# Optimization experiments

Hardware: AMD Instinct MI355X
Metric: run time of the kernel (lower is better)

Reference implementation:

```python
import jax, jax.numpy as jnp
import numpy as np

B, N, ATTR, H, OUT, STEPS = 8, 4096, 16, 64, 1, 8


def setup_inputs() -> dict:
    key = jax.random.key(0)
    ks = jax.random.split(key, 12)
    attr_matrix = jax.random.normal(ks[0], (B, N, ATTR), jnp.float32)
    adj_matrix = (jax.random.uniform(ks[1], (B, N, N)) < 0.01).astype(jnp.float32)
    s = float(1.0 / np.sqrt(H))
    u = lambda k, shape: jax.random.uniform(k, shape, jnp.float32, -s, s)
    Wi = jax.random.normal(ks[2], (H, ATTR), jnp.float32) * float(np.sqrt(2.0 / ATTR))  # kaiming
    bi = jnp.zeros((H,), jnp.float32)
    Wz = u(ks[3], (H, 3 * H)); bz = u(ks[4], (H,))
    Wr = u(ks[5], (H, 3 * H)); br = u(ks[6], (H,))
    Wh = u(ks[7], (H, 3 * H)); bh = u(ks[8], (H,))
    Wo = jax.random.normal(ks[9], (OUT, H), jnp.float32) * float(np.sqrt(2.0 / (H + OUT)))  # xavier
    bo = jnp.zeros((OUT,), jnp.float32)
    return dict(attr_matrix=attr_matrix, adj_matrix=adj_matrix, Wi=Wi, bi=bi,
                Wz=Wz, bz=bz, Wr=Wr, br=br, Wh=Wh, bh=bh, Wo=Wo, bo=bo)


def reference(attr_matrix, adj_matrix, Wi, bi, Wz, bz, Wr, br, Wh, bh, Wo, bo):
    # initial node states: (B, N, H)
    h = jax.nn.relu(attr_matrix @ Wi.T + bi)
    A_in = adj_matrix
    A_out = jnp.swapaxes(adj_matrix, -1, -2)
    for _ in range(STEPS):
        a_in = jnp.einsum('bij,bjh->bih', A_in, h)
        a_out = jnp.einsum('bij,bjh->bih', A_out, h)
        inp = jnp.concatenate([a_in, a_out], axis=-1)           # (B, N, 2H)
        xs = jnp.concatenate([inp, h], axis=-1)                  # (B, N, 3H)
        z = jax.nn.sigmoid(xs @ Wz.T + bz)
        r = jax.nn.sigmoid(xs @ Wr.T + br)
        hn = jnp.tanh(jnp.concatenate([inp, r * h], axis=-1) @ Wh.T + bh)
        h = (1.0 - z) * h + z * hn
    return h @ Wo.T + bo  # (B, N, OUT)
```

## Files before the change

kernel.cpp:

```cpp
#include <hip/hip_runtime.h>
#include <hip/hip_fp16.h>
#include <stdint.h>

#define BB 8
#define NN 4096
#define ATTRD 16
#define HD 64
#define STEPS 8
#define NODES (BB*NN)
#define ECAP 96
#define KPAD 196

typedef _Float16 half8 __attribute__((ext_vector_type(8)));
typedef float floatx4 __attribute__((ext_vector_type(4)));
typedef unsigned long long ull;

__global__ void init_h_kernel(const float* __restrict__ attr, const float* __restrict__ Wi,
                              const float* __restrict__ bi, float* __restrict__ h,
                              __half* __restrict__ h16) {
    int idx = blockIdx.x * blockDim.x + threadIdx.x;
    if (idx >= (NODES + 1) * HD) return;
    if (idx >= NODES * HD) {
        h16[idx] = __float2half(0.f);
        return;
    }
    int node = idx >> 6, l = idx & 63;
    const float* a = attr + node * ATTRD;
    const float* w = Wi + l * ATTRD;
    float acc = bi[l];
#pragma unroll
    for (int k = 0; k < ATTRD; k++) acc += a[k] * w[k];
    float r = acc > 0.f ? acc : 0.f;
    h[idx] = r;
    h16[idx] = __float2half(r);
}

__global__ void wprep_kernel(const float* __restrict__ Wz, const float* __restrict__ Wr,
                             const float* __restrict__ Wh,
                             _Float16* __restrict__ wf_hi, _Float16* __restrict__ wf_lo) {
    int t = blockIdx.x * blockDim.x + threadIdx.x;
    if (t >= 3 * 4 * 6 * 64 * 8) return;
    int mat = t / 12288, rem = t % 12288;
    int tile = rem / 3072, rem2 = rem % 3072;
    int kc = rem2 / 512, rem3 = rem2 % 512;
    int lane = rem3 / 8, j = rem3 % 8;
    int k = kc * 32 + (lane >> 4) * 8 + j;
    int och = tile * 16 + (lane & 15);
    const float* W = (mat == 0) ? Wz : (mat == 1) ? Wr : Wh;
    float v = W[och * 192 + k];
    _Float16 hi = (_Float16)v;
    wf_hi[t] = hi;
    wf_lo[t] = (_Float16)(v - (float)hi);
}

__global__ __launch_bounds__(256) void count_rows_kernel(const float4* __restrict__ A4,
                                                         int* __restrict__ cnt_in,
                                                         int* __restrict__ edge_in) {
    int wave = threadIdx.x >> 6, l = threadIdx.x & 63;
    int row = blockIdx.x * 4 + wave;
    const float4* rp = A4 + (size_t)row * 1024;
    ull mask_lt = (l == 63) ? ~0ull >> 1 : ((1ull << (l + 1)) - 1) >> 1;
    float4 v[16];
#pragma unroll
    for (int t = 0; t < 16; t++) v[t] = rp[t * 64 + l];
    int colbase = (row >> 12) << 12;
    int run = 0;
    int* erow = edge_in + row * ECAP;
#pragma unroll
    for (int t = 0; t < 16; t++) {
        ull b0 = __ballot(v[t].x != 0.f);
        ull b1 = __ballot(v[t].y != 0.f);
        ull b2 = __ballot(v[t].z != 0.f);
        ull b3 = __ballot(v[t].w != 0.f);
        int pre = __popcll(b0 & mask_lt) + __popcll(b1 & mask_lt) +
                  __popcll(b2 & mask_lt) + __popcll(b3 & mask_lt);
        float vv[4] = {v[t].x, v[t].y, v[t].z, v[t].w};
        int jbase = (t * 64 + l) * 4;
        int inner = 0;
#pragma unroll
        for (int q = 0; q < 4; q++) {
            if (vv[q] != 0.f) {
                int slot = run + pre + inner;
                if (slot < ECAP) erow[slot] = colbase | (jbase + q);
                inner++;
            }
        }
        run += __popcll(b0) + __popcll(b1) + __popcll(b2) + __popcll(b3);
    }
    if (l == 0) cnt_in[row] = run;
}

__global__ __launch_bounds__(256) void transpose_kernel(const int* __restrict__ cnt_in,
                                                        const int* __restrict__ edge_in,
                                                        int* __restrict__ cnt_out,
                                                        int* __restrict__ edge_out) {
    int wave = threadIdx.x >> 6, l = threadIdx.x & 63;
    int row = blockIdx.x * 4 + wave;
    int n = cnt_in[row]; if (n > ECAP) n = ECAP;
    for (int s = l; s < n; s += 64) {
        int j = edge_in[row * ECAP + s];
        int s2 = atomicAdd(&cnt_out[j], 1);
        if (s2 < ECAP) edge_out[j * ECAP + s2] = row;
    }
}

__global__ __launch_bounds__(256) void aggregate_kernel(
        const uint4* __restrict__ h4, const float* __restrict__ h,
        const int* __restrict__ cnt_in, const int* __restrict__ edge_in,
        const int* __restrict__ cnt_out, const int* __restrict__ edge_out,
        float* __restrict__ xs) {
    int bid = blockIdx.x;
    int batch = bid & 7;
    int group = bid >> 3;
    int wave = threadIdx.x >> 6;
    int pair = group * 4 + wave;
    int node = (batch << 12) + (pair >> 1);
    int dir = pair & 1;
    int l = threadIdx.x & 63;
    int sub = l >> 3;
    int part = l & 7;
    int n = dir ? cnt_out[node] : cnt_in[node];
    if (n > ECAP) n = ECAP;
    const int* erow = (dir ? edge_out : edge_in) + node * ECAP;
    int e0 = erow[l];
    int e1 = erow[64 + (l & 31)];
    float a0 = 0.f, a1 = 0.f, a2 = 0.f, a3 = 0.f, a4 = 0.f, a5 = 0.f, a6 = 0.f, a7 = 0.f;
    for (int s = 0; s < n; s += 8) {
        int il = s + sub;
        int gidx = (il < 64) ? __shfl(e0, il) : __shfl(e1, il - 64);
        gidx = (il < n) ? gidx : NODES;
        uint4 g = h4[(gidx << 3) | part];
        float2 p0 = __half22float2(*(__half2*)&g.x);
        float2 p1 = __half22float2(*(__half2*)&g.y);
        float2 p2 = __half22float2(*(__half2*)&g.z);
        float2 p3 = __half22float2(*(__half2*)&g.w);
        a0 += p0.x; a1 += p0.y; a2 += p1.x; a3 += p1.y;
        a4 += p2.x; a5 += p2.y; a6 += p3.x; a7 += p3.y;
    }
#pragma unroll
    for (int off = 8; off < 64; off <<= 1) {
        a0 += __shfl_xor(a0, off); a1 += __shfl_xor(a1, off);
        a2 += __shfl_xor(a2, off); a3 += __shfl_xor(a3, off);
        a4 += __shfl_xor(a4, off); a5 += __shfl_xor(a5, off);
        a6 += __shfl_xor(a6, off); a7 += __shfl_xor(a7, off);
    }
    if (l < 8) {
        float4 s0 = {a0, a1, a2, a3};
        float4 s1 = {a4, a5, a6, a7};
        float* dst = xs + node * 192 + dir * 64 + l * 8;
        *(float4*)dst = s0;
        *(float4*)(dst + 4) = s1;
    }
    if (dir == 0) xs[node * 192 + 128 + l] = h[(node << 6) | l];
}

__global__ __launch_bounds__(256) void gate_kernel(
        const float* __restrict__ xs_g,
        const _Float16* __restrict__ wf_hi, const _Float16* __restrict__ wf_lo,
        const float* __restrict__ bz, const float* __restrict__ br,
        const float* __restrict__ bh,
        float* __restrict__ h, __half* __restrict__ h16) {
    __shared__ float xs_t[16][KPAD];
    int bid = blockIdx.x;
    int base = ((bid & 7) << 12) | ((bid >> 3) << 4);
    int tid = threadIdx.x;
    {
        const float4* src = (const float4*)(xs_g + base * 192);
#pragma unroll
        for (int i = 0; i < 3; i++) {
            int idx = tid + i * 256;
            float4 v = src[idx];
            int nl = idx / 48, kb = (idx % 48) * 4;
            *(float4*)&xs_t[nl][kb] = v;
        }
    }
    __syncthreads();
    int wave = tid >> 6, lane = tid & 63;
    int m = lane & 15, q = lane >> 4;
    int ch = wave * 16 + m;
    const half8* WH = (const half8*)wf_hi;
    const half8* WL = (const half8*)wf_lo;

    floatx4 accz = {0.f, 0.f, 0.f, 0.f};
    floatx4 accr = {0.f, 0.f, 0.f, 0.f};
#pragma unroll
    for (int kc = 0; kc < 6; kc++) {
        const float* xr = &xs_t[m][kc * 32 + q * 8];
        float4 xa = *(const float4*)xr;
        float4 xb = *(const float4*)(xr + 4);
        float xv[8] = {xa.x, xa.y, xa.z, xa.w, xb.x, xb.y, xb.z, xb.w};
        half8 ahi, alo;
#pragma unroll
        for (int j = 0; j < 8; j++) {
            _Float16 hj = (_Float16)xv[j];
            ahi[j] = hj;
            alo[j] = (_Float16)(xv[j] - (float)hj);
        }
        half8 bzh = WH[((0 * 4 + wave) * 6 + kc) * 64 + lane];
        half8 bzl = WL[((0 * 4 + wave) * 6 + kc) * 64 + lane];
        half8 brh = WH[((1 * 4 + wave) * 6 + kc) * 64 + lane];
        half8 brl = WL[((1 * 4 + wave) * 6 + kc) * 64 + lane];
        accz = __builtin_amdgcn_mfma_f32_16x16x32_f16(ahi, bzh, accz, 0, 0, 0);
        accz = __builtin_amdgcn_mfma_f32_16x16x32_f16(alo, bzh, accz, 0, 0, 0);
        accz = __builtin_amdgcn_mfma_f32_16x16x32_f16(ahi, bzl, accz, 0, 0, 0);
        accr = __builtin_amdgcn_mfma_f32_16x16x32_f16(ahi, brh, accr, 0, 0, 0);
        accr = __builtin_amdgcn_mfma_f32_16x16x32_f16(alo, brh, accr, 0, 0, 0);
        accr = __builtin_amdgcn_mfma_f32_16x16x32_f16(ahi, brl, accr, 0, 0, 0);
    }
    float bzv = bz[ch], brv = br[ch], bhv = bh[ch];
    float zreg[4], hvreg[4], rh[4];
#pragma unroll
    for (int rg = 0; rg < 4; rg++) {
        int nl = q * 4 + rg;
        float z = 1.f / (1.f + __expf(-(accz[rg] + bzv)));
        float r = 1.f / (1.f + __expf(-(accr[rg] + brv)));
        float hv = xs_t[nl][128 + ch];
        zreg[rg] = z; hvreg[rg] = hv; rh[rg] = r * hv;
    }
    __syncthreads();
#pragma unroll
    for (int rg = 0; rg < 4; rg++) xs_t[q * 4 + rg][128 + ch] = rh[rg];
    __syncthreads();

    floatx4 acch = {0.f, 0.f, 0.f, 0.f};
#pragma unroll
    for (int kc = 0; kc < 6; kc++) {
        const float* xr = &xs_t[m][kc * 32 + q * 8];
        float4 xa = *(const float4*)xr;
        float4 xb = *(const float4*)(xr + 4);
        float xv[8] = {xa.x, xa.y, xa.z, xa.w, xb.x, xb.y, xb.z, xb.w};
        half8 ahi, alo;
#pragma unroll
        for (int j = 0; j < 8; j++) {
            _Float16 hj = (_Float16)xv[j];
            ahi[j] = hj;
            alo[j] = (_Float16)(xv[j] - (float)hj);
        }
        half8 bhh = WH[((2 * 4 + wave) * 6 + kc) * 64 + lane];
        half8 bhl = WL[((2 * 4 + wave) * 6 + kc) * 64 + lane];
        acch = __builtin_amdgcn_mfma_f32_16x16x32_f16(ahi, bhh, acch, 0, 0, 0);
        acch = __builtin_amdgcn_mfma_f32_16x16x32_f16(alo, bhh, acch, 0, 0, 0);
        acch = __builtin_amdgcn_mfma_f32_16x16x32_f16(ahi, bhl, acch, 0, 0, 0);
    }
    __syncthreads();
#pragma unroll
    for (int rg = 0; rg < 4; rg++) {
        int nl = q * 4 + rg;
        float pre = acch[rg] + bhv;
        float th = 2.f / (1.f + __expf(-2.f * pre)) - 1.f;
        float hv = hvreg[rg];
        xs_t[nl][ch] = hv + zreg[rg] * (th - hv);
    }
    __syncthreads();
    {
        int f = tid * 4;
        int nl = f >> 6, c = f & 63;
        float4 v = *(const float4*)&xs_t[nl][c];
        int gi = ((base + nl) << 6) | c;
        *(float4*)&h[gi] = v;
        __half2 p0 = {__float2half(v.x), __float2half(v.y)};
        __half2 p1 = {__float2half(v.z), __float2half(v.w)};
        *(__half2*)&h16[gi] = p0;
        *(__half2*)&h16[gi + 2] = p1;
    }
}

__global__ void out_kernel(const float* __restrict__ h, const float* __restrict__ Wo,
                           const float* __restrict__ bo, float* __restrict__ out) {
    int wid = (blockIdx.x * blockDim.x + threadIdx.x) >> 6;
    int l = threadIdx.x & 63;
    if (wid >= NODES) return;
    float p = h[(wid << 6) | l] * Wo[l];
#pragma unroll
    for (int off = 32; off > 0; off >>= 1) p += __shfl_down(p, off);
    if (l == 0) out[wid] = p + bo[0];
}

extern "C" void kernel_launch(void* const* d_in, const int* in_sizes, int n_in,
                              void* d_out, int out_size, void* d_ws, size_t ws_size,
                              hipStream_t stream) {
    const float* attr = (const float*)d_in[0];
    const float* adj  = (const float*)d_in[1];
    const float* Wi   = (const float*)d_in[2];
    const float* bi   = (const float*)d_in[3];
    const float* Wz   = (const float*)d_in[4];
    const float* bz   = (const float*)d_in[5];
    const float* Wr   = (const float*)d_in[6];
    const float* br   = (const float*)d_in[7];
    const float* Wh   = (const float*)d_in[8];
    const float* bh   = (const float*)d_in[9];
    const float* Wo   = (const float*)d_in[10];
    const float* bo   = (const float*)d_in[11];
    float* out = (float*)d_out;

    char* ws = (char*)d_ws;
    size_t off = 0;
    auto carve = [&](size_t bytes) { void* p = ws + off; off = (off + bytes + 255) & ~(size_t)255; return p; };
    float* h      = (float*)carve((size_t)NODES * HD * 4);
    __half* h16   = (__half*)carve((size_t)(NODES + 1) * HD * 2);
    float* xs     = (float*)carve((size_t)NODES * 192 * 4);
    _Float16* wf_hi = (_Float16*)carve(3 * 4 * 6 * 64 * 8 * 2);
    _Float16* wf_lo = (_Float16*)carve(3 * 4 * 6 * 64 * 8 * 2);
    int* cnt_in   = (int*)carve((size_t)NODES * 4);
    int* cnt_out  = (int*)carve((size_t)NODES * 4);
    int* edge_in  = (int*)carve((size_t)NODES * ECAP * 4);
    int* edge_out = (int*)carve((size_t)NODES * ECAP * 4);

    hipMemsetAsync(cnt_out, 0, (size_t)NODES * 4, stream);

    init_h_kernel<<<((NODES + 1) * HD + 255) / 256, 256, 0, stream>>>(attr, Wi, bi, h, h16);
    wprep_kernel<<<(3 * 4 * 6 * 64 * 8 + 255) / 256, 256, 0, stream>>>(Wz, Wr, Wh, wf_hi, wf_lo);
    count_rows_kernel<<<NODES / 4, 256, 0, stream>>>((const float4*)adj, cnt_in, edge_in);
    transpose_kernel<<<NODES / 4, 256, 0, stream>>>(cnt_in, edge_in, cnt_out, edge_out);

    for (int step = 0; step < STEPS; ++step) {
        aggregate_kernel<<<NODES * 2 * 64 / 256, 256, 0, stream>>>(
            (const uint4*)h16, h, cnt_in, edge_in, cnt_out, edge_out, xs);
        gate_kernel<<<NODES / 16, 256, 0, stream>>>(xs, wf_hi, wf_lo, bz, br, bh, h, h16);
    }
    out_kernel<<<NODES * HD / 256, 256, 0, stream>>>(h, Wo, bo, out);
}
```

Baseline: 1.225 ms.

## Fuse adjacency transpose into row scan and merge in/out aggregation per wave

The separate transpose kernel is removed: the row-scan kernel now issues the atomic increments that build the outgoing edge lists directly while it scans the dense adjacency. The aggregate kernel now handles both directions for a node in one wave, interleaving the two gathers and halving the grid. This saves a launch and a re-read of edge lists, and raises memory-level parallelism per wave, at the cost of more registers and idle lanes when in/out degrees differ.

```diff
diff --git a/kernel.cpp b/kernel.cpp
--- a/kernel.cpp
+++ b/kernel.cpp
@@ -55,7 +55,9 @@
 
 __global__ __launch_bounds__(256) void count_rows_kernel(const float4* __restrict__ A4,
                                                          int* __restrict__ cnt_in,
-                                                         int* __restrict__ edge_in) {
+                                                         int* __restrict__ edge_in,
+                                                         int* __restrict__ cnt_out,
+                                                         int* __restrict__ edge_out) {
     int wave = threadIdx.x >> 6, l = threadIdx.x & 63;
     int row = blockIdx.x * 4 + wave;
     const float4* rp = A4 + (size_t)row * 1024;
@@ -80,28 +82,17 @@
 #pragma unroll
         for (int q = 0; q < 4; q++) {
             if (vv[q] != 0.f) {
+                int col = colbase | (jbase + q);
                 int slot = run + pre + inner;
-                if (slot < ECAP) erow[slot] = colbase | (jbase + q);
+                if (slot < ECAP) erow[slot] = col;
                 inner++;
+                int s2 = atomicAdd(&cnt_out[col], 1);
+                if (s2 < ECAP) edge_out[col * ECAP + s2] = row;
             }
         }
         run += __popcll(b0) + __popcll(b1) + __popcll(b2) + __popcll(b3);
     }
     if (l == 0) cnt_in[row] = run;
-}
-
-__global__ __launch_bounds__(256) void transpose_kernel(const int* __restrict__ cnt_in,
-                                                        const int* __restrict__ edge_in,
-                                                        int* __restrict__ cnt_out,
-                                                        int* __restrict__ edge_out) {
-    int wave = threadIdx.x >> 6, l = threadIdx.x & 63;
-    int row = blockIdx.x * 4 + wave;
-    int n = cnt_in[row]; if (n > ECAP) n = ECAP;
-    for (int s = l; s < n; s += 64) {
-        int j = edge_in[row * ECAP + s];
-        int s2 = atomicAdd(&cnt_out[j], 1);
-        if (s2 < ECAP) edge_out[j * ECAP + s2] = row;
-    }
 }
 
 __global__ __launch_bounds__(256) void aggregate_kernel(
@@ -113,45 +104,63 @@
     int batch = bid & 7;
     int group = bid >> 3;
     int wave = threadIdx.x >> 6;
-    int pair = group * 4 + wave;
-    int node = (batch << 12) + (pair >> 1);
-    int dir = pair & 1;
+    int node = (batch << 12) + group * 4 + wave;
     int l = threadIdx.x & 63;
     int sub = l >> 3;
     int part = l & 7;
-    int n = dir ? cnt_out[node] : cnt_in[node];
-    if (n > ECAP) n = ECAP;
-    const int* erow = (dir ? edge_out : edge_in) + node * ECAP;
-    int e0 = erow[l];
-    int e1 = erow[64 + (l & 31)];
-    float a0 = 0.f, a1 = 0.f, a2 = 0.f, a3 = 0.f, a4 = 0.f, a5 = 0.f, a6 = 0.f, a7 = 0.f;
-    for (int s = 0; s < n; s += 8) {
+    int ni = cnt_in[node];  if (ni > ECAP) ni = ECAP;
+    int no = cnt_out[node]; if (no > ECAP) no = ECAP;
+    const int* ei = edge_in + node * ECAP;
+    const int* eo = edge_out + node * ECAP;
+    int ei0 = ei[l], ei1 = ei[64 + (l & 31)];
+    int eo0 = eo[l], eo1 = eo[64 + (l & 31)];
+    float ai0 = 0.f, ai1 = 0.f, ai2 = 0.f, ai3 = 0.f, ai4 = 0.f, ai5 = 0.f, ai6 = 0.f, ai7 = 0.f;
+    float ao0 = 0.f, ao1 = 0.f, ao2 = 0.f, ao3 = 0.f, ao4 = 0.f, ao5 = 0.f, ao6 = 0.f, ao7 = 0.f;
+    int nmax = ni > no ? ni : no;
+    for (int s = 0; s < nmax; s += 8) {
         int il = s + sub;
-        int gidx = (il < 64) ? __shfl(e0, il) : __shfl(e1, il - 64);
-        gidx = (il < n) ? gidx : NODES;
-        uint4 g = h4[(gidx << 3) | part];
-        float2 p0 = __half22float2(*(__half2*)&g.x);
-        float2 p1 = __half22float2(*(__half2*)&g.y);
-        float2 p2 = __half22float2(*(__half2*)&g.z);
-        float2 p3 = __half22float2(*(__half2*)&g.w);
-        a0 += p0.x; a1 += p0.y; a2 += p1.x; a3 += p1.y;
-        a4 += p2.x; a5 += p2.y; a6 += p3.x; a7 += p3.y;
+        int gi = (il < 64) ? __shfl(ei0, il) : __shfl(ei1, il - 64);
+        int go = (il < 64) ? __shfl(eo0, il) : __shfl(eo1, il - 64);
+        gi = (il < ni) ? gi : NODES;
+        go = (il < no) ? go : NODES;
+        uint4 gA = h4[(gi << 3) | part];
+        uint4 gB = h4[(go << 3) | part];
+        float2 pA0 = __half22float2(*(__half2*)&gA.x);
+        float2 pA1 = __half22float2(*(__half2*)&gA.y);
+        float2 pA2 = __half22float2(*(__half2*)&gA.z);
+        float2 pA3 = __half22float2(*(__half2*)&gA.w);
+        ai0 += pA0.x; ai1 += pA0.y; ai2 += pA1.x; ai3 += pA1.y;
+        ai4 += pA2.x; ai5 += pA2.y; ai6 += pA3.x; ai7 += pA3.y;
+        float2 pB0 = __half22float2(*(__half2*)&gB.x);
+        float2 pB1 = __half22float2(*(__half2*)&gB.y);
+        float2 pB2 = __half22float2(*(__half2*)&gB.z);
+        float2 pB3 = __half22float2(*(__half2*)&gB.w);
+        ao0 += pB0.x; ao1 += pB0.y; ao2 += pB1.x; ao3 += pB1.y;
+        ao4 += pB2.x; ao5 += pB2.y; ao6 += pB3.x; ao7 += pB3.y;
     }
 #pragma unroll
     for (int off = 8; off < 64; off <<= 1) {
-        a0 += __shfl_xor(a0, off); a1 += __shfl_xor(a1, off);
-        a2 += __shfl_xor(a2, off); a3 += __shfl_xor(a3, off);
-        a4 += __shfl_xor(a4, off); a5 += __shfl_xor(a5, off);
-        a6 += __shfl_xor(a6, off); a7 += __shfl_xor(a7, off);
+        ai0 += __shfl_xor(ai0, off); ai1 += __shfl_xor(ai1, off);
+        ai2 += __shfl_xor(ai2, off); ai3 += __shfl_xor(ai3, off);
+        ai4 += __shfl_xor(ai4, off); ai5 += __shfl_xor(ai5, off);
+        ai6 += __shfl_xor(ai6, off); ai7 += __shfl_xor(ai7, off);
+        ao0 += __shfl_xor(ao0, off); ao1 += __shfl_xor(ao1, off);
+        ao2 += __shfl_xor(ao2, off); ao3 += __shfl_xor(ao3, off);
+        ao4 += __shfl_xor(ao4, off); ao5 += __shfl_xor(ao5, off);
+        ao6 += __shfl_xor(ao6, off); ao7 += __shfl_xor(ao7, off);
     }
     if (l < 8) {
-        float4 s0 = {a0, a1, a2, a3};
-        float4 s1 = {a4, a5, a6, a7};
-        float* dst = xs + node * 192 + dir * 64 + l * 8;
-        *(float4*)dst = s0;
-        *(float4*)(dst + 4) = s1;
-    }
-    if (dir == 0) xs[node * 192 + 128 + l] = h[(node << 6) | l];
+        float* dst = xs + node * 192;
+        float4 si0 = {ai0, ai1, ai2, ai3};
+        float4 si1 = {ai4, ai5, ai6, ai7};
+        float4 so0 = {ao0, ao1, ao2, ao3};
+        float4 so1 = {ao4, ao5, ao6, ao7};
+        *(float4*)(dst + l * 8)      = si0;
+        *(float4*)(dst + l * 8 + 4)  = si1;
+        *(float4*)(dst + 64 + l * 8)     = so0;
+        *(float4*)(dst + 64 + l * 8 + 4) = so1;
+    }
+    xs[node * 192 + 128 + l] = h[(node << 6) | l];
 }
 
 __global__ __launch_bounds__(256) void gate_kernel(
@@ -310,11 +319,11 @@
 
     init_h_kernel<<<((NODES + 1) * HD + 255) / 256, 256, 0, stream>>>(attr, Wi, bi, h, h16);
     wprep_kernel<<<(3 * 4 * 6 * 64 * 8 + 255) / 256, 256, 0, stream>>>(Wz, Wr, Wh, wf_hi, wf_lo);
-    count_rows_kernel<<<NODES / 4, 256, 0, stream>>>((const float4*)adj, cnt_in, edge_in);
-    transpose_kernel<<<NODES / 4, 256, 0, stream>>>(cnt_in, edge_in, cnt_out, edge_out);
+    count_rows_kernel<<<NODES / 4, 256, 0, stream>>>((const float4*)adj, cnt_in, edge_in,
+                                                     cnt_out, edge_out);
 
     for (int step = 0; step < STEPS; ++step) {
-        aggregate_kernel<<<NODES * 2 * 64 / 256, 256, 0, stream>>>(
+        aggregate_kernel<<<NODES / 4, 256, 0, stream>>>(
             (const uint4*)h16, h, cnt_in, edge_in, cnt_out, edge_out, xs);
         gate_kernel<<<NODES / 16, 256, 0, stream>>>(xs, wf_hi, wf_lo, bz, br, bh, h, h16);
     }
```

Result: faster. 1.181 ms (-3.6%).
